# Kernel tuning notes

Measured on AMD Instinct MI355X. Metric: run time of the kernel, lower is better.

The kernel has to match this reference:

```python
import jax, jax.numpy as jnp
import numpy as np

EPS = 1e-5
N_HEADS = 8

def layer_norm(x, g, b):
    mu = x.mean(-1, keepdims=True)
    var = ((x - mu) ** 2).mean(-1, keepdims=True)
    return (x - mu) * jax.lax.rsqrt(var + EPS) * g + b

def rotate_half(x):
    d = x.shape[-1] // 2
    return jnp.concatenate([-x[..., d:], x[..., :d]], axis=-1)

def setup_inputs() -> dict:
    key = jax.random.key(0)
    ks = jax.random.split(key, 6)
    b, n, m, h, dh = 4, 512, 8192, N_HEADS, 16
    dim = h * dh
    s = dim ** -0.5
    return {
        "x": jax.random.normal(ks[0], (b, n, dim), jnp.float32),
        "mem_kv": jax.random.normal(ks[1], (b, h, m, 2 * dh), jnp.float32),
        "w_q": jax.random.normal(ks[2], (dim, dim), jnp.float32) * s,
        "w_kv": jax.random.normal(ks[3], (2 * dim, dim), jnp.float32) * s,
        "w_out": jax.random.normal(ks[4], (dim, dim), jnp.float32) * s,
        "b_out": jnp.zeros((dim,), jnp.float32),
        "g1": jnp.ones((dim,), jnp.float32),
        "b1": jnp.zeros((dim,), jnp.float32),
        "g2": jnp.ones((dim,), jnp.float32),
        "b2": jnp.zeros((dim,), jnp.float32),
    }

def reference(x, mem_kv, w_q, w_kv, w_out, b_out, g1, b1, g2, b2):
    b, n, dim = x.shape
    h = N_HEADS
    dh = dim // h
    # pre-norm + projections
    x_ = layer_norm(x, g1, b1)
    q = (x_ @ w_q.T).reshape(b, n, h, dh).transpose(0, 2, 1, 3)          # [b,h,n,dh]
    kv = (x_ @ w_kv.T).reshape(b, n, h, 2 * dh).transpose(0, 2, 1, 3)    # [b,h,n,2dh]
    mem_kv = jnp.concatenate([mem_kv, kv], axis=2)                        # growing cache
    k, v = jnp.split(mem_kv, 2, axis=-1)                                  # [b,h,j,dh] each
    q = q * dh ** -0.5
    # rotary embeddings (SinusoidalEmbeddings over k length, q uses trailing n positions)
    j = k.shape[2]
    inv_freq = 1.0 / (10000.0 ** (jnp.arange(0, dh, 2, dtype=jnp.float32) / dh))
    fr = jnp.arange(j, dtype=jnp.float32)[:, None] * inv_freq[None, :]
    freqs = jnp.concatenate([fr, fr], axis=-1)                            # [j, dh]
    cos, sin = jnp.cos(freqs), jnp.sin(freqs)
    q = q * cos[-n:] + rotate_half(q) * sin[-n:]
    k = k * cos + rotate_half(k) * sin
    # full attention of new chunk over cache (forward_simple, inference)
    sim = jnp.einsum('bhie,bhje->bhij', q, k)
    attn = jax.nn.softmax(sim, axis=-1)
    hv = jnp.einsum('bhij,bhje->bhie', attn, v)
    hv = hv.transpose(0, 2, 1, 3).reshape(b, n, dim) + x                  # residual
    out = layer_norm(hv, g2, b2) @ w_out.T + b_out + hv                   # out proj + residual
    return out, mem_kv
```

## Files before the change

### kernel.cpp

```cpp
#include <hip/hip_runtime.h>

#define B 4
#define N 512
#define M 8192
#define H 8
#define DH 16
#define DIM 128
#define J (M + N)
#define LN10000_DIV8 1.1512925465f
#define LOG2E 1.44269504f

typedef _Float16 f16;
typedef _Float16 half4 __attribute__((ext_vector_type(4)));
typedef _Float16 half8 __attribute__((ext_vector_type(8)));
typedef __fp16 fp16x2 __attribute__((ext_vector_type(2)));
typedef float f32x4 __attribute__((ext_vector_type(4)));

#if __has_builtin(__builtin_amdgcn_exp2f)
#define EXP2(x) __builtin_amdgcn_exp2f(x)
#else
#define EXP2(x) exp2f(x)
#endif

union PK { fp16x2 v; unsigned int u; };

__device__ __forceinline__ half8 pack8(float a, float b, float c, float d,
                                       float e, float f, float g, float h) {
#if __has_builtin(__builtin_amdgcn_cvt_pkrtz)
    union { unsigned int u[4]; half8 h8; } r;
    PK p0, p1, p2, p3;
    p0.v = __builtin_amdgcn_cvt_pkrtz(a, b);
    p1.v = __builtin_amdgcn_cvt_pkrtz(c, d);
    p2.v = __builtin_amdgcn_cvt_pkrtz(e, f);
    p3.v = __builtin_amdgcn_cvt_pkrtz(g, h);
    r.u[0] = p0.u; r.u[1] = p1.u; r.u[2] = p2.u; r.u[3] = p3.u;
    return r.h8;
#else
    half8 r = { (f16)a, (f16)b, (f16)c, (f16)d, (f16)e, (f16)f, (f16)g, (f16)h };
    return r;
#endif
}

#define WS_KROT 0ull
#define WS_VT   8912896ull
#define WS_QROT 17825792ull
#define WS_HV   18350080ull
#define WS_XN   18874368ull

union V4  { f16 h[4];  uint2 u; };

__device__ __forceinline__ half8 cvt8(const float* p) {
    float4 a = *(const float4*)p, b = *(const float4*)(p + 4);
    half8 h = { (f16)a.x, (f16)a.y, (f16)a.z, (f16)a.w,
                (f16)b.x, (f16)b.y, (f16)b.z, (f16)b.w };
    return h;
}

__global__ void __launch_bounds__(256) ln_kernel(
    const float* __restrict__ x, const float* __restrict__ g1,
    const float* __restrict__ b1, f16* __restrict__ xn16)
{
    int wave = threadIdx.x >> 6, lane = threadIdx.x & 63;
    int token = blockIdx.x * 4 + wave;
    float v0 = x[(size_t)token * DIM + lane];
    float v1 = x[(size_t)token * DIM + lane + 64];
    float s = v0 + v1;
    for (int off = 32; off; off >>= 1) s += __shfl_xor(s, off, 64);
    float mu = s * (1.0f / DIM);
    float d0 = v0 - mu, d1 = v1 - mu;
    float vs = d0 * d0 + d1 * d1;
    for (int off = 32; off; off >>= 1) vs += __shfl_xor(vs, off, 64);
    float rs = rsqrtf(vs * (1.0f / DIM) + 1e-5f);
    xn16[(size_t)token * DIM + lane]      = (f16)(d0 * rs * g1[lane]      + b1[lane]);
    xn16[(size_t)token * DIM + lane + 64] = (f16)(d1 * rs * g1[lane + 64] + b1[lane + 64]);
}

__global__ void __launch_bounds__(256) prep_proj_kernel(
    const float4* __restrict__ src, float4* __restrict__ dstv,
    f16* __restrict__ krot, f16* __restrict__ vt,
    const f16* __restrict__ xn16, const float* __restrict__ wq,
    const float* __restrict__ wkv, f16* __restrict__ qrot)
{
    if (blockIdx.x < 768) {
        float* out_mem = (float*)dstv;
        int id = blockIdx.x * 4 + (threadIdx.x >> 6);
        int lane = threadIdx.x & 63;
        int ttile = id & 127, ctile = id >> 7;
        int token0 = ttile * 16;
        int col = lane & 15, quad = lane >> 4;

        const float* wbase = (ctile < 8) ? (wq + (size_t)(ctile * 16 + col) * DIM)
                                         : (wkv + (size_t)((ctile - 8) * 16 + col) * DIM);
        const f16* abase = xn16 + (size_t)(token0 + col) * DIM + quad * 8;

        f32x4 acc = {0.f, 0.f, 0.f, 0.f};
        #pragma unroll
        for (int kb = 0; kb < 4; kb++) {
            half8 a = *(const half8*)(abase + kb * 32);
            half8 w = cvt8(wbase + kb * 32 + quad * 8);
            acc = __builtin_amdgcn_mfma_f32_16x16x32_f16(a, w, acc, 0, 0, 0);
        }

        int e = col, r8 = e & 7;
        float f = __expf(-(float)r8 * LN10000_DIV8);
        int kt = ctile - 8;
        int head = (ctile < 8) ? ctile : (kt >> 1);
        int isV  = (ctile >= 8) ? (kt & 1) : 0;

        #pragma unroll
        for (int r = 0; r < 4; r++) {
            int tok = token0 + quad * 4 + r;
            int b = tok >> 9, i = tok & (N - 1);
            int bhh = b * H + head;
            float self = acc[r];
            float prt = __shfl_xor(self, 8, 64);

            if (ctile < 8) {
                float ang = (float)(M + i) * f;
                float sn, cs; __sincosf(ang, &sn, &cs);
                float rv = (self * cs + ((e < 8) ? -prt : prt) * sn) * (0.25f * LOG2E);
                qrot[((size_t)bhh * N + i) * 16 + e] = (f16)rv;
            } else if (!isV) {
                out_mem[((size_t)bhh * J + M + i) * 32 + e] = self;
                float ang = (float)(M + i) * f;
                float sn, cs; __sincosf(ang, &sn, &cs);
                float rv = self * cs + ((e < 8) ? -prt : prt) * sn;
                int jpos = M + i;
                int tilei = jpos >> 5, jj = jpos & 31;
                int col4 = (jj >> 3) * 4 + (jj & 3), frag = (jj >> 2) & 1;
                krot[(size_t)bhh * J * 16 + (size_t)tilei * 512 +
                     (e >> 2) * 128 + col4 * 8 + frag * 4 + (e & 3)] = (f16)rv;
            } else {
                out_mem[((size_t)bhh * J + M + i) * 32 + 16 + e] = self;
                vt[(size_t)bhh * 16 * J + (size_t)e * J + M + i] = (f16)self;
            }
        }
    } else {
        __shared__ float tile[64][33];
        int bid = blockIdx.x - 768;
        int bh = bid >> 7;
        int j0 = (bid & 127) * 64;
        int t = threadIdx.x;

        #pragma unroll
        for (int rep = 0; rep < 2; rep++) {
            int idx = t + rep * 256;
            int row = idx >> 3, c4 = idx & 7;
            float4 v = src[((size_t)bh * M + j0 + row) * 8 + c4];
            f32x4 vv = { v.x, v.y, v.z, v.w };
            __builtin_nontemporal_store(vv,
                (f32x4*)dstv + ((size_t)bh * J + j0 + row) * 8 + c4);
            tile[row][c4 * 4 + 0] = v.x; tile[row][c4 * 4 + 1] = v.y;
            tile[row][c4 * 4 + 2] = v.z; tile[row][c4 * 4 + 3] = v.w;
        }
        __syncthreads();

        if (t < 128) {
            int row = t >> 1, rh = t & 1;
            int j = j0 + row;
            float lo4[4], hi4[4];
            #pragma unroll
            for (int i = 0; i < 4; i++) {
                int r = rh * 4 + i;
                float ang = (float)j * __expf(-(float)r * LN10000_DIV8);
                float sn, cs; __sincosf(ang, &sn, &cs);
                float lo = tile[row][r], hi = tile[row][r + 8];
                lo4[i] = lo * cs - hi * sn;
                hi4[i] = hi * cs + lo * sn;
            }
            int tilei = j >> 5, jj = j & 31;
            int col4 = (jj >> 3) * 4 + (jj & 3), frag = (jj >> 2) & 1;
            f16* base = krot + (size_t)bh * J * 16 + (size_t)tilei * 512 + col4 * 8 + frag * 4;
            V4 wl, wh;
            #pragma unroll
            for (int i = 0; i < 4; i++) { wl.h[i] = (f16)lo4[i]; wh.h[i] = (f16)hi4[i]; }
            *(uint2*)(base + rh * 128)       = wl.u;
            *(uint2*)(base + (2 + rh) * 128) = wh.u;
        }
        {
            int dh = t >> 4, c0 = (t & 15) * 4;
            V4 vv;
            #pragma unroll
            for (int i = 0; i < 4; i++) vv.h[i] = (f16)tile[c0 + i][16 + dh];
            *(uint2*)(vt + (size_t)bh * 16 * J + (size_t)dh * J + j0 + c0) = vv.u;
        }
    }
}

__global__ void __launch_bounds__(1024) attn_kernel(
    const f16* __restrict__ krot, const f16* __restrict__ vt,
    const f16* __restrict__ qrot, f16* __restrict__ hvw)
{
    __shared__ float sacc[16][2][256];
    __shared__ float sl[16][2][16];
    int bh = blockIdx.x & 31;
    int q0 = (blockIdx.x >> 5) * 32;
    int wave = threadIdx.x >> 6, lane = threadIdx.x & 63;
    int col = lane & 15, quad = lane >> 4;

    const f16* vb = vt + (size_t)bh * 16 * J + (size_t)col * J;
    half4 qfa = *(const half4*)(qrot + ((size_t)bh * N + q0 + col) * 16 + quad * 4);
    half4 qfb = *(const half4*)(qrot + ((size_t)bh * N + q0 + 16 + col) * 16 + quad * 4);

    int jstart = wave * (J / 16);
    const f16* kptr = krot + (size_t)bh * J * 16 + (size_t)jstart * 16 + lane * 8;
    const f16* vptr = vb + jstart + quad * 8;

    f32x4 acca = {0.f, 0.f, 0.f, 0.f};
    f32x4 accb = {0.f, 0.f, 0.f, 0.f};
    f32x4 accla = {0.f, 0.f, 0.f, 0.f};
    f32x4 acclb = {0.f, 0.f, 0.f, 0.f};
    const f32x4 zero = {0.f, 0.f, 0.f, 0.f};
    const half8 ones = { (f16)1.f, (f16)1.f, (f16)1.f, (f16)1.f,
                         (f16)1.f, (f16)1.f, (f16)1.f, (f16)1.f };

    #pragma unroll 2
    for (int it = 0; it < 17; ++it) {
        half8 kf8 = *(const half8*)kptr;
        half8 vf  = *(const half8*)vptr;
        kptr += 512; vptr += 32;
        half4 kf0 = __builtin_shufflevector(kf8, kf8, 0, 1, 2, 3);
        half4 kf1 = __builtin_shufflevector(kf8, kf8, 4, 5, 6, 7);
        f32x4 s0a = __builtin_amdgcn_mfma_f32_16x16x16f16(kf0, qfa, zero, 0, 0, 0);
        f32x4 s1a = __builtin_amdgcn_mfma_f32_16x16x16f16(kf1, qfa, zero, 0, 0, 0);
        f32x4 s0b = __builtin_amdgcn_mfma_f32_16x16x16f16(kf0, qfb, zero, 0, 0, 0);
        f32x4 s1b = __builtin_amdgcn_mfma_f32_16x16x16f16(kf1, qfb, zero, 0, 0, 0);

        float a0 = EXP2(s0a[0]), a1 = EXP2(s0a[1]), a2 = EXP2(s0a[2]), a3 = EXP2(s0a[3]);
        float a4 = EXP2(s1a[0]), a5 = EXP2(s1a[1]), a6 = EXP2(s1a[2]), a7 = EXP2(s1a[3]);
        float b0 = EXP2(s0b[0]), b1 = EXP2(s0b[1]), b2 = EXP2(s0b[2]), b3 = EXP2(s0b[3]);
        float b4 = EXP2(s1b[0]), b5 = EXP2(s1b[1]), b6 = EXP2(s1b[2]), b7 = EXP2(s1b[3]);
        half8 pfa = pack8(a0, a1, a2, a3, a4, a5, a6, a7);
        half8 pfb = pack8(b0, b1, b2, b3, b4, b5, b6, b7);
        acca  = __builtin_amdgcn_mfma_f32_16x16x32_f16(pfa, vf,   acca,  0, 0, 0);
        accla = __builtin_amdgcn_mfma_f32_16x16x32_f16(pfa, ones, accla, 0, 0, 0);
        accb  = __builtin_amdgcn_mfma_f32_16x16x32_f16(pfb, vf,   accb,  0, 0, 0);
        acclb = __builtin_amdgcn_mfma_f32_16x16x32_f16(pfb, ones, acclb, 0, 0, 0);
    }

    if (col == 0) {
        #pragma unroll
        for (int r = 0; r < 4; r++) {
            sl[wave][0][quad * 4 + r] = accla[r];
            sl[wave][1][quad * 4 + r] = acclb[r];
        }
    }
    #pragma unroll
    for (int r = 0; r < 4; r++) {
        sacc[wave][0][(quad * 4 + r) * 16 + col] = acca[r];
        sacc[wave][1][(quad * 4 + r) * 16 + col] = accb[r];
    }
    __syncthreads();

    if (threadIdx.x < 512) {
        int t = threadIdx.x;
        int qt = t >> 8, ql = (t >> 4) & 15, c = t & 15;
        float o = 0.f, lt = 0.f;
        #pragma unroll
        for (int w = 0; w < 16; w++) {
            o  += sacc[w][qt][ql * 16 + c];
            lt += sl[w][qt][ql];
        }
        int b = bh >> 3, h = bh & 7;
        hvw[((size_t)(b * N) + q0 + qt * 16 + ql) * DIM + h * DH + c] = (f16)(o / lt);
    }
}

__global__ void __launch_bounds__(256) final_kernel(
    const f16* __restrict__ hvw, const float* __restrict__ x,
    const float* __restrict__ wout, const float* __restrict__ bout,
    const float* __restrict__ g2, const float* __restrict__ b2v,
    float* __restrict__ out)
{
    __shared__ f16 xn2[16][136];
    __shared__ float hres[16][132];
    int token0 = (blockIdx.x >> 1) * 16;
    int half = blockIdx.x & 1;
    int wave = threadIdx.x >> 6, lane = threadIdx.x & 63;

    #pragma unroll
    for (int tt = 0; tt < 4; tt++) {
        int tl = wave * 4 + tt;
        int token = token0 + tl;
        float h0 = (float)hvw[(size_t)token * DIM + lane]      + x[(size_t)token * DIM + lane];
        float h1 = (float)hvw[(size_t)token * DIM + lane + 64] + x[(size_t)token * DIM + lane + 64];
        float s = h0 + h1;
        for (int off = 32; off; off >>= 1) s += __shfl_xor(s, off, 64);
        float mu = s * (1.0f / DIM);
        float d0 = h0 - mu, d1 = h1 - mu;
        float vs = d0 * d0 + d1 * d1;
        for (int off = 32; off; off >>= 1) vs += __shfl_xor(vs, off, 64);
        float rs = rsqrtf(vs * (1.0f / DIM) + 1e-5f);
        xn2[tl][lane]      = (f16)(d0 * rs * g2[lane]      + b2v[lane]);
        xn2[tl][lane + 64] = (f16)(d1 * rs * g2[lane + 64] + b2v[lane + 64]);
        hres[tl][lane] = h0; hres[tl][lane + 64] = h1;
    }
    __syncthreads();

    int col = lane & 15, quad = lane >> 4;
    int ct = half * 4 + wave;
    int cg = ct * 16 + col;
    const float* wrow = wout + (size_t)cg * DIM;
    f32x4 acc = {0.f, 0.f, 0.f, 0.f};
    #pragma unroll
    for (int kb = 0; kb < 4; kb++) {
        half8 a = *(const half8*)(&xn2[col][kb * 32 + quad * 8]);
        half8 w = cvt8(wrow + kb * 32 + quad * 8);
        acc = __builtin_amdgcn_mfma_f32_16x16x32_f16(a, w, acc, 0, 0, 0);
    }
    float bo = bout[cg];
    #pragma unroll
    for (int r = 0; r < 4; r++) {
        int tl = quad * 4 + r;
        out[(size_t)(token0 + tl) * DIM + cg] = acc[r] + bo + hres[tl][cg];
    }
}

extern "C" void kernel_launch(void* const* d_in, const int* in_sizes, int n_in,
                              void* d_out, int out_size, void* d_ws, size_t ws_size,
                              hipStream_t stream)
{
    const float* x      = (const float*)d_in[0];
    const float* mem_kv = (const float*)d_in[1];
    const float* wq     = (const float*)d_in[2];
    const float* wkv    = (const float*)d_in[3];
    const float* wout   = (const float*)d_in[4];
    const float* bout   = (const float*)d_in[5];
    const float* g1     = (const float*)d_in[6];
    const float* b1     = (const float*)d_in[7];
    const float* g2     = (const float*)d_in[8];
    const float* b2     = (const float*)d_in[9];

    float* out = (float*)d_out;
    float* out_mem = out + (size_t)B * N * DIM;

    f16* krot = (f16*)((char*)d_ws + WS_KROT);
    f16* vt   = (f16*)((char*)d_ws + WS_VT);
    f16* qrot = (f16*)((char*)d_ws + WS_QROT);
    f16* hvw  = (f16*)((char*)d_ws + WS_HV);
    f16* xn16 = (f16*)((char*)d_ws + WS_XN);

    hipLaunchKernelGGL(ln_kernel, dim3(512), dim3(256), 0, stream,
                       x, g1, b1, xn16);
    hipLaunchKernelGGL(prep_proj_kernel, dim3(4864), dim3(256), 0, stream,
                       (const float4*)mem_kv, (float4*)out_mem, krot, vt,
                       xn16, wq, wkv, qrot);
    hipLaunchKernelGGL(attn_kernel, dim3(512), dim3(1024), 0, stream,
                       krot, vt, qrot, hvw);
    hipLaunchKernelGGL(final_kernel, dim3(256), dim3(256), 0, stream,
                       hvw, x, wout, bout, g2, b2, out);
}
```

Before: 138.2 us.

## Fuse input layernorm into projection kernel, add MFMA priority and nontemporal loads

Removes the separate layernorm launch. Each projection wave now recomputes the layernorm for its 16 tokens into shared memory, so the fp16 normalized activations no longer make a round trip through global memory. This adds redundant LN work, since every column tile recomputes the same tokens. The change also makes the cache-copy loads nontemporal and wraps the attention MFMA groups in s_setprio to favour matrix issue.

```diff
diff --git a/kernel.cpp b/kernel.cpp
--- a/kernel.cpp
+++ b/kernel.cpp
@@ -45,7 +45,6 @@
 #define WS_VT   8912896ull
 #define WS_QROT 17825792ull
 #define WS_HV   18350080ull
-#define WS_XN   18874368ull
 
 union V4  { f16 h[4];  uint2 u; };
 
@@ -56,49 +55,54 @@
     return h;
 }
 
-__global__ void __launch_bounds__(256) ln_kernel(
+__global__ void __launch_bounds__(256) prep_proj_kernel(
+    const f32x4* __restrict__ src, float4* __restrict__ dstv,
+    f16* __restrict__ krot, f16* __restrict__ vt,
     const float* __restrict__ x, const float* __restrict__ g1,
-    const float* __restrict__ b1, f16* __restrict__ xn16)
-{
-    int wave = threadIdx.x >> 6, lane = threadIdx.x & 63;
-    int token = blockIdx.x * 4 + wave;
-    float v0 = x[(size_t)token * DIM + lane];
-    float v1 = x[(size_t)token * DIM + lane + 64];
-    float s = v0 + v1;
-    for (int off = 32; off; off >>= 1) s += __shfl_xor(s, off, 64);
-    float mu = s * (1.0f / DIM);
-    float d0 = v0 - mu, d1 = v1 - mu;
-    float vs = d0 * d0 + d1 * d1;
-    for (int off = 32; off; off >>= 1) vs += __shfl_xor(vs, off, 64);
-    float rs = rsqrtf(vs * (1.0f / DIM) + 1e-5f);
-    xn16[(size_t)token * DIM + lane]      = (f16)(d0 * rs * g1[lane]      + b1[lane]);
-    xn16[(size_t)token * DIM + lane + 64] = (f16)(d1 * rs * g1[lane + 64] + b1[lane + 64]);
-}
-
-__global__ void __launch_bounds__(256) prep_proj_kernel(
-    const float4* __restrict__ src, float4* __restrict__ dstv,
-    f16* __restrict__ krot, f16* __restrict__ vt,
-    const f16* __restrict__ xn16, const float* __restrict__ wq,
+    const float* __restrict__ b1, const float* __restrict__ wq,
     const float* __restrict__ wkv, f16* __restrict__ qrot)
 {
+    __shared__ __attribute__((aligned(16))) char smem[17408];
+
     if (blockIdx.x < 768) {
+        f16 (*xnl)[136] = (f16 (*)[136])smem;
         float* out_mem = (float*)dstv;
-        int id = blockIdx.x * 4 + (threadIdx.x >> 6);
-        int lane = threadIdx.x & 63;
+        int w = threadIdx.x >> 6, lane = threadIdx.x & 63;
+        int id = blockIdx.x * 4 + w;
         int ttile = id & 127, ctile = id >> 7;
         int token0 = ttile * 16;
         int col = lane & 15, quad = lane >> 4;
 
+        {
+            float g1a = g1[lane], g1b = g1[lane + 64];
+            float b1a = b1[lane], b1b = b1[lane + 64];
+            #pragma unroll 4
+            for (int tt = 0; tt < 16; tt++) {
+                int token = token0 + tt;
+                float v0 = x[(size_t)token * DIM + lane];
+                float v1 = x[(size_t)token * DIM + lane + 64];
+                float s = v0 + v1;
+                for (int off = 32; off; off >>= 1) s += __shfl_xor(s, off, 64);
+                float mu = s * (1.0f / DIM);
+                float d0 = v0 - mu, d1 = v1 - mu;
+                float vs = d0 * d0 + d1 * d1;
+                for (int off = 32; off; off >>= 1) vs += __shfl_xor(vs, off, 64);
+                float rs = rsqrtf(vs * (1.0f / DIM) + 1e-5f);
+                xnl[w * 16 + tt][lane]      = (f16)(d0 * rs * g1a + b1a);
+                xnl[w * 16 + tt][lane + 64] = (f16)(d1 * rs * g1b + b1b);
+            }
+        }
+
         const float* wbase = (ctile < 8) ? (wq + (size_t)(ctile * 16 + col) * DIM)
                                          : (wkv + (size_t)((ctile - 8) * 16 + col) * DIM);
-        const f16* abase = xn16 + (size_t)(token0 + col) * DIM + quad * 8;
+        const f16* arow = &xnl[w * 16 + col][quad * 8];
 
         f32x4 acc = {0.f, 0.f, 0.f, 0.f};
         #pragma unroll
         for (int kb = 0; kb < 4; kb++) {
-            half8 a = *(const half8*)(abase + kb * 32);
-            half8 w = cvt8(wbase + kb * 32 + quad * 8);
-            acc = __builtin_amdgcn_mfma_f32_16x16x32_f16(a, w, acc, 0, 0, 0);
+            half8 a = *(const half8*)(arow + kb * 32);
+            half8 wv = cvt8(wbase + kb * 32 + quad * 8);
+            acc = __builtin_amdgcn_mfma_f32_16x16x32_f16(a, wv, acc, 0, 0, 0);
         }
 
         int e = col, r8 = e & 7;
@@ -136,7 +140,7 @@
             }
         }
     } else {
-        __shared__ float tile[64][33];
+        float (*tile)[33] = (float (*)[33])smem;
         int bid = blockIdx.x - 768;
         int bh = bid >> 7;
         int j0 = (bid & 127) * 64;
@@ -146,12 +150,11 @@
         for (int rep = 0; rep < 2; rep++) {
             int idx = t + rep * 256;
             int row = idx >> 3, c4 = idx & 7;
-            float4 v = src[((size_t)bh * M + j0 + row) * 8 + c4];
-            f32x4 vv = { v.x, v.y, v.z, v.w };
-            __builtin_nontemporal_store(vv,
+            f32x4 v = __builtin_nontemporal_load(src + ((size_t)bh * M + j0 + row) * 8 + c4);
+            __builtin_nontemporal_store(v,
                 (f32x4*)dstv + ((size_t)bh * J + j0 + row) * 8 + c4);
-            tile[row][c4 * 4 + 0] = v.x; tile[row][c4 * 4 + 1] = v.y;
-            tile[row][c4 * 4 + 2] = v.z; tile[row][c4 * 4 + 3] = v.w;
+            tile[row][c4 * 4 + 0] = v[0]; tile[row][c4 * 4 + 1] = v[1];
+            tile[row][c4 * 4 + 2] = v[2]; tile[row][c4 * 4 + 3] = v[3];
         }
         __syncthreads();
 
@@ -221,10 +224,12 @@
         kptr += 512; vptr += 32;
         half4 kf0 = __builtin_shufflevector(kf8, kf8, 0, 1, 2, 3);
         half4 kf1 = __builtin_shufflevector(kf8, kf8, 4, 5, 6, 7);
+        __builtin_amdgcn_s_setprio(1);
         f32x4 s0a = __builtin_amdgcn_mfma_f32_16x16x16f16(kf0, qfa, zero, 0, 0, 0);
         f32x4 s1a = __builtin_amdgcn_mfma_f32_16x16x16f16(kf1, qfa, zero, 0, 0, 0);
         f32x4 s0b = __builtin_amdgcn_mfma_f32_16x16x16f16(kf0, qfb, zero, 0, 0, 0);
         f32x4 s1b = __builtin_amdgcn_mfma_f32_16x16x16f16(kf1, qfb, zero, 0, 0, 0);
+        __builtin_amdgcn_s_setprio(0);
 
         float a0 = EXP2(s0a[0]), a1 = EXP2(s0a[1]), a2 = EXP2(s0a[2]), a3 = EXP2(s0a[3]);
         float a4 = EXP2(s1a[0]), a5 = EXP2(s1a[1]), a6 = EXP2(s1a[2]), a7 = EXP2(s1a[3]);
@@ -232,10 +237,12 @@
         float b4 = EXP2(s1b[0]), b5 = EXP2(s1b[1]), b6 = EXP2(s1b[2]), b7 = EXP2(s1b[3]);
         half8 pfa = pack8(a0, a1, a2, a3, a4, a5, a6, a7);
         half8 pfb = pack8(b0, b1, b2, b3, b4, b5, b6, b7);
+        __builtin_amdgcn_s_setprio(1);
         acca  = __builtin_amdgcn_mfma_f32_16x16x32_f16(pfa, vf,   acca,  0, 0, 0);
         accla = __builtin_amdgcn_mfma_f32_16x16x32_f16(pfa, ones, accla, 0, 0, 0);
         accb  = __builtin_amdgcn_mfma_f32_16x16x32_f16(pfb, vf,   accb,  0, 0, 0);
         acclb = __builtin_amdgcn_mfma_f32_16x16x32_f16(pfb, ones, acclb, 0, 0, 0);
+        __builtin_amdgcn_s_setprio(0);
     }
 
     if (col == 0) {
@@ -338,13 +345,10 @@
     f16* vt   = (f16*)((char*)d_ws + WS_VT);
     f16* qrot = (f16*)((char*)d_ws + WS_QROT);
     f16* hvw  = (f16*)((char*)d_ws + WS_HV);
-    f16* xn16 = (f16*)((char*)d_ws + WS_XN);
-
-    hipLaunchKernelGGL(ln_kernel, dim3(512), dim3(256), 0, stream,
-                       x, g1, b1, xn16);
+
     hipLaunchKernelGGL(prep_proj_kernel, dim3(4864), dim3(256), 0, stream,
-                       (const float4*)mem_kv, (float4*)out_mem, krot, vt,
-                       xn16, wq, wkv, qrot);
+                       (const f32x4*)mem_kv, (float4*)out_mem, krot, vt,
+                       x, g1, b1, wq, wkv, qrot);
     hipLaunchKernelGGL(attn_kernel, dim3(512), dim3(1024), 0, stream,
                        krot, vt, qrot, hvw);
     hipLaunchKernelGGL(final_kernel, dim3(256), dim3(256), 0, stream,
```

Measured after the change: 139.9 us. Within noise of the previous version (+1.3%).
